# Performance work log

Hardware: AMD Instinct MI355X
Metric: run time of the kernel (lower is better)

## Reference

```python
import jax, jax.numpy as jnp
import numpy as np

MIN_NORM = 1e-15
EPS = 1e-5
C_CURV = 1.0  # args.c

def _norm(x):
    return jnp.clip(jnp.linalg.norm(x, axis=-1, keepdims=True), MIN_NORM)

def artanh(x):
    x = jnp.clip(x, -1.0 + EPS, 1.0 - EPS)
    return 0.5 * (jnp.log1p(x) - jnp.log1p(-x))

def proj(x, c):
    # clip points to stay strictly inside the Poincare ball
    norm = _norm(x)
    maxnorm = (1.0 - EPS) / jnp.sqrt(c)
    return jnp.where(norm > maxnorm, x / norm * maxnorm, x)

def expmap0(u, c):
    sqrt_c = jnp.sqrt(c)
    u_norm = _norm(u)
    return jnp.tanh(sqrt_c * u_norm) * u / (sqrt_c * u_norm)

def logmap0(p, c):
    sqrt_c = jnp.sqrt(c)
    p_norm = _norm(p)
    return artanh(sqrt_c * p_norm) * p / (sqrt_c * p_norm)

def mobius_add(x, y, c):
    x2 = jnp.sum(x * x, axis=-1, keepdims=True)
    y2 = jnp.sum(y * y, axis=-1, keepdims=True)
    xy = jnp.sum(x * y, axis=-1, keepdims=True)
    num = (1.0 + 2.0 * c * xy + c * y2) * x + (1.0 - c * x2) * y
    denom = 1.0 + 2.0 * c * xy + c * c * x2 * y2
    return num / jnp.clip(denom, MIN_NORM)

def mobius_matvec(W, x, c):
    sqrt_c = jnp.sqrt(c)
    x_norm = _norm(x)
    mx = x @ W.T
    mx_norm = _norm(mx)
    return jnp.tanh(mx_norm / x_norm * artanh(sqrt_c * x_norm)) * mx / (mx_norm * sqrt_c)

def poincare_dist(x, y, c):
    sqrt_c = jnp.sqrt(c)
    d = _norm(mobius_add(-x, y, c))[..., 0]
    return 2.0 / sqrt_c * artanh(sqrt_c * d)

def hgnn_layer(h, adj, W, b, c):
    # HypLinear: mobius matvec + hyperbolic bias
    mv = proj(mobius_matvec(W, h, c), c)
    hyp_b = proj(expmap0(b, c), c)
    h = proj(mobius_add(mv, hyp_b, c), c)
    # HypAgg: aggregate in tangent space at origin
    h = proj(expmap0(adj @ logmap0(h, c), c), c)
    # HypAct: relu in tangent space
    return proj(expmap0(jax.nn.relu(logmap0(h, c)), c), c)

def setup_inputs() -> dict:
    key = jax.random.key(0)
    ks = jax.random.split(key, 10)
    N, D, C, NC, NODE_C, L = 8192, 128, 64, 7, 7, 4
    x = jax.random.normal(ks[0], (N, D), jnp.float32)
    adj = jax.random.uniform(ks[1], (N, N), jnp.float32) / N  # row-stochastic-ish dense adjacency
    graph_indicator = jax.random.randint(ks[2], (N,), 0, 1)
    W_conv = jax.random.normal(ks[3], (L, D, D), jnp.float32) / np.sqrt(D)
    b_conv = jax.random.normal(ks[4], (L, D), jnp.float32) * 0.01
    centroids = jax.random.normal(ks[5], (C, D), jnp.float32) * 0.1
    W_mlp = jax.random.normal(ks[6], (NC, C), jnp.float32) * 0.1
    b_mlp = jnp.zeros((NC,), jnp.float32)
    W_mlp1 = jax.random.normal(ks[7], (NODE_C, D), jnp.float32) * 0.1
    b_mlp1 = jnp.zeros((NODE_C,), jnp.float32)
    return {"x": x, "adj": adj, "graph_indicator": graph_indicator,
            "W_conv": W_conv, "b_conv": b_conv, "centroids": centroids,
            "W_mlp": W_mlp, "b_mlp": b_mlp, "W_mlp1": W_mlp1, "b_mlp1": b_mlp1}

def reference(x, adj, graph_indicator, W_conv, b_conv, centroids, W_mlp, b_mlp, W_mlp1, b_mlp1):
    c = C_CURV
    # proj_tan0 is identity for PoincareBall
    h = proj(expmap0(x, c), c)
    # 2 residual blocks, each with 2 HGNN layers; shortcut is identity (in_dim == out_dim)
    for blk in range(2):
        res = h
        for j in range(2):
            idx = blk * 2 + j
            h = hgnn_layer(h, adj, W_conv[idx], b_conv[idx], c)
        h = h + res  # Euclidean residual, as in the source
    # CentroidDistance: pairwise hyperbolic distance [N, C]
    node_centroid_dist = poincare_dist(h[:, None, :], centroids[None, :, :], c)
    readout = jnp.mean(node_centroid_dist, axis=0, keepdims=True)  # [1, C]
    h_r = logmap0(readout, c)  # proj_tan0(logmap0(.)) -> identity proj_tan0
    logits = jax.nn.softmax(h_r @ W_mlp.T + b_mlp, axis=0)[None]        # [1,1,NC]
    h1 = logmap0(h, c)
    logits_node = jax.nn.softmax(h1 @ W_mlp1.T + b_mlp1, axis=0)[None]  # [1,N,node_classes]
    return (logits, logits_node, h_r)
```

## Files before the change

kernel.cpp:

```cpp
#include <hip/hip_runtime.h>

#define MIN_NORM 1e-15f
#define EPSV 1e-5f
#define MAXN (1.0f - EPSV)
#define NN 8192
#define DD 128

typedef unsigned short u16;
typedef __bf16 bf16x8 __attribute__((ext_vector_type(8)));
typedef float f32x4 __attribute__((ext_vector_type(4)));

__device__ __forceinline__ float wave_sum(float v) {
#pragma unroll
  for (int off = 32; off > 0; off >>= 1) v += __shfl_xor(v, off, 64);
  return v;
}

__device__ __forceinline__ float artanh_f(float x) {
  x = fminf(fmaxf(x, -1.0f + EPSV), 1.0f - EPSV);
  return 0.5f * (log1pf(x) - log1pf(-x));
}

__device__ __forceinline__ u16 f2bf(float f) {
  unsigned u = __float_as_uint(f);
  unsigned r = (u + 0x7fffu + ((u >> 16) & 1u)) >> 16;
  return (u16)r;
}
__device__ __forceinline__ float bf2f(u16 b) { return __uint_as_float(((unsigned)b) << 16); }

__device__ __forceinline__ void gload16(const u16* g, u16* l) {
  __builtin_amdgcn_global_load_lds((const __attribute__((address_space(1))) void*)(g),
                                   (__attribute__((address_space(3))) void*)(l), 16, 0, 0);
}

template <bool TILED>
__global__ __launch_bounds__(256) void gemm_bt(const u16* __restrict__ A,
                                               const u16* __restrict__ Bt,
                                               float* __restrict__ Cp,
                                               int M, int K, int KC) {
  __shared__ __align__(16) u16 Ash[2 * 64 * 64];
  __shared__ __align__(16) u16 Bsh[2 * 128 * 64];

  const int tid = threadIdx.x;
  const int lane = tid & 63;
  const int w = tid >> 6;
  const int wm = w >> 1, wn = w & 1;
  const int lrow = lane & 15;
  const int lq = lane >> 4;
  const int m0 = blockIdx.x * 64;
  const int kk0 = blockIdx.y * KC;
  const int kt0 = kk0 >> 6;
  const int bxK = blockIdx.x * (K >> 6);

  const int srow = lane >> 3;
  const int spc = lane & 7;

  const u16* Ap = A + (TILED ? 0 : (size_t)m0 * K);

  f32x4 acc[2][4];
#pragma unroll
  for (int a = 0; a < 2; a++)
#pragma unroll
    for (int b = 0; b < 4; b++)
#pragma unroll
      for (int r = 0; r < 4; r++) acc[a][b][r] = 0.0f;

#define STAGE(bf, tkt, kk)                                                     \
  do {                                                                         \
    if constexpr (TILED) {                                                     \
      const u16* at = A + (((size_t)(bxK + (tkt))) << 12) + (lane << 3);       \
      _Pragma("unroll") for (int ii = 0; ii < 2; ii++)                         \
        gload16(at + ((ii * 4 + w) << 9), &Ash[(bf) * 4096 + ((ii * 4 + w) << 9)]); \
      const u16* bt2 = Bt + (((size_t)(tkt)) << 13) + (lane << 3);             \
      _Pragma("unroll") for (int ii = 0; ii < 4; ii++)                         \
        gload16(bt2 + ((ii * 4 + w) << 9), &Bsh[(bf) * 8192 + ((ii * 4 + w) << 9)]); \
    } else {                                                                   \
      _Pragma("unroll") for (int ii = 0; ii < 2; ii++) {                       \
        int rw = ((ii * 4 + w) << 3) + srow;                                   \
        gload16(Ap + (size_t)rw * K + (kk) + ((spc ^ (rw & 7)) << 3),          \
                &Ash[(bf) * 4096 + ((ii * 4 + w) << 9)]);                      \
      }                                                                        \
      _Pragma("unroll") for (int ii = 0; ii < 4; ii++) {                       \
        int rw = ((ii * 4 + w) << 3) + srow;                                   \
        gload16(Bt + (size_t)rw * K + (kk) + ((spc ^ (rw & 7)) << 3),          \
                &Bsh[(bf) * 8192 + ((ii * 4 + w) << 9)]);                      \
      }                                                                        \
    }                                                                          \
  } while (0)

  const int nt = KC >> 6;
  STAGE(0, kt0, kk0);

  for (int t = 0; t < nt; t++) {
    const int cur = t & 1;
    __syncthreads();
    if (t + 1 < nt) STAGE(cur ^ 1, kt0 + t + 1, kk0 + (t + 1) * 64);

    const int abase = cur * 4096, bbase = cur * 8192;
#pragma unroll
    for (int ks = 0; ks < 2; ks++) {
      const int lc = ks * 4 + lq;
      bf16x8 af[2], bfr[4];
#pragma unroll
      for (int ti = 0; ti < 2; ti++) {
        int r = wm * 32 + ti * 16 + lrow;
        af[ti] = *(const bf16x8*)&Ash[abase + r * 64 + ((lc ^ (r & 7)) << 3)];
      }
#pragma unroll
      for (int tj = 0; tj < 4; tj++) {
        int n = wn * 64 + tj * 16 + lrow;
        bfr[tj] = *(const bf16x8*)&Bsh[bbase + n * 64 + ((lc ^ (n & 7)) << 3)];
      }
#pragma unroll
      for (int ti = 0; ti < 2; ti++)
#pragma unroll
        for (int tj = 0; tj < 4; tj++)
          acc[ti][tj] = __builtin_amdgcn_mfma_f32_16x16x32_bf16(af[ti], bfr[tj], acc[ti][tj], 0, 0, 0);
    }
  }
#undef STAGE

  float* C = Cp + (size_t)blockIdx.y * M * 128;
#pragma unroll
  for (int ti = 0; ti < 2; ti++)
#pragma unroll
    for (int tj = 0; tj < 4; tj++)
#pragma unroll
      for (int r = 0; r < 4; r++) {
        int row = m0 + wm * 32 + ti * 16 + lq * 4 + r;
        int col = wn * 64 + tj * 16 + lrow;
        C[(size_t)row * 128 + col] = acc[ti][tj][r];
      }
}

__global__ __launch_bounds__(256) void cvt_tile(const float* __restrict__ src,
                                                u16* __restrict__ dst) {
  int tid = threadIdx.x;
  int xb = blockIdx.x;
  int kg = blockIdx.y;
  int ch = tid & 63;
  int rs = tid >> 6;
#pragma unroll
  for (int rr = 0; rr < 16; rr++) {
    int row = rr * 4 + rs;
    int gk = kg * 512 + ch * 8;
    const float* s = src + (size_t)(xb * 64 + row) * NN + gk;
    float4 a = *(const float4*)s;
    float4 b = *(const float4*)(s + 4);
    ushort4 d0, d1;
    d0.x = f2bf(a.x); d0.y = f2bf(a.y); d0.z = f2bf(a.z); d0.w = f2bf(a.w);
    d1.x = f2bf(b.x); d1.y = f2bf(b.y); d1.z = f2bf(b.z); d1.w = f2bf(b.w);
    u16* d = dst + (((size_t)(xb * 128 + (gk >> 6))) << 12) + row * 64 +
             ((((gk >> 3) & 7) ^ (row & 7)) << 3);
    *(ushort4*)d = d0;
    *(ushort4*)(d + 4) = d1;
  }
}

__global__ void build_wt(const float* __restrict__ W, u16* __restrict__ Wt2) {
  int idx = blockIdx.x * 256 + threadIdx.x;
  if (idx >= 4 * 128 * 128) return;
  int layer = idx >> 14;
  int n = (idx >> 7) & 127;
  int k = idx & 127;
  float e = W[idx];
  u16 hi = f2bf(e);
  u16 lo = f2bf(e - bf2f(hi));
  u16* base = Wt2 + (size_t)layer * 128 * 384 + (size_t)n * 384;
  base[k] = hi;
  base[128 + k] = hi;
  base[256 + k] = lo;
}

__device__ __forceinline__ void write_split(u16* hs, int i, int lane, float v0, float v1) {
  u16* row = hs + (size_t)i * 384;
  u16 h0 = f2bf(v0), h1 = f2bf(v1);
  u16 l0 = f2bf(v0 - bf2f(h0)), l1 = f2bf(v1 - bf2f(h1));
  row[lane] = h0;         row[lane + 64] = h1;
  row[128 + lane] = l0;   row[128 + 64 + lane] = l1;
  row[256 + lane] = h0;   row[256 + 64 + lane] = h1;
}

__global__ __launch_bounds__(64) void rowwise_init(const float* __restrict__ x,
                                                   float* __restrict__ h,
                                                   float* __restrict__ res,
                                                   u16* __restrict__ hsplit) {
  int i = blockIdx.x, lane = threadIdx.x;
  const float* xr = x + (size_t)i * DD;
  float a0 = xr[lane], a1 = xr[lane + 64];
  float n = fmaxf(sqrtf(wave_sum(a0 * a0 + a1 * a1)), MIN_NORM);
  float g = tanhf(n) / n;
  float y0 = g * a0, y1 = g * a1;
  float pn = fmaxf(sqrtf(wave_sum(y0 * y0 + y1 * y1)), MIN_NORM);
  float s = pn > MAXN ? MAXN / pn : 1.0f;
  y0 *= s; y1 *= s;
  size_t base = (size_t)i * DD;
  h[base + lane] = y0;   h[base + lane + 64] = y1;
  res[base + lane] = y0; res[base + lane + 64] = y1;
  write_split(hsplit, i, lane, y0, y1);
}

__global__ __launch_bounds__(64) void rowwise_mid(const float* __restrict__ h,
                                                  const float* __restrict__ P,
                                                  const float* __restrict__ bvec,
                                                  u16* __restrict__ uT2) {
  int i = blockIdx.x, lane = threadIdx.x;
  size_t base = (size_t)i * DD;
  const float* hr = h + base;
  float h0 = hr[lane], h1 = hr[lane + 64];
  float m0 = 0.f, m1 = 0.f;
#pragma unroll
  for (int sk = 0; sk < 3; sk++) {
    const float* p = P + (size_t)sk * NN * DD + base;
    m0 += p[lane];
    m1 += p[lane + 64];
  }
  float xn = fmaxf(sqrtf(wave_sum(h0 * h0 + h1 * h1)), MIN_NORM);
  float mn = fmaxf(sqrtf(wave_sum(m0 * m0 + m1 * m1)), MIN_NORM);
  float t = tanhf(mn / xn * artanh_f(xn));
  float v0 = t * m0 / mn, v1 = t * m1 / mn;
  float pn = fmaxf(sqrtf(wave_sum(v0 * v0 + v1 * v1)), MIN_NORM);
  float sc = pn > MAXN ? MAXN / pn : 1.0f;
  v0 *= sc; v1 *= sc;
  float b0 = bvec[lane], b1 = bvec[lane + 64];
  float bn = fmaxf(sqrtf(wave_sum(b0 * b0 + b1 * b1)), MIN_NORM);
  float gb = tanhf(bn) / bn;
  float e0 = gb * b0, e1 = gb * b1;
  float en = fmaxf(sqrtf(wave_sum(e0 * e0 + e1 * e1)), MIN_NORM);
  float sb = en > MAXN ? MAXN / en : 1.0f;
  e0 *= sb; e1 *= sb;
  float x2 = wave_sum(v0 * v0 + v1 * v1);
  float y2 = wave_sum(e0 * e0 + e1 * e1);
  float xy = wave_sum(v0 * e0 + v1 * e1);
  float ca = 1.0f + 2.0f * xy + y2;
  float cb = 1.0f - x2;
  float den = fmaxf(1.0f + 2.0f * xy + x2 * y2, MIN_NORM);
  float t0 = (ca * v0 + cb * e0) / den, t1 = (ca * v1 + cb * e1) / den;
  float tn = fmaxf(sqrtf(wave_sum(t0 * t0 + t1 * t1)), MIN_NORM);
  float st = tn > MAXN ? MAXN / tn : 1.0f;
  t0 *= st; t1 *= st;
  float pn2 = fmaxf(sqrtf(wave_sum(t0 * t0 + t1 * t1)), MIN_NORM);
  float gl = artanh_f(pn2) / pn2;
  u16* tb = uT2 + (((size_t)(i >> 6)) << 13);
  int c8 = (i >> 3) & 7, k7 = i & 7;
  tb[lane * 64 + (((c8) ^ (lane & 7)) << 3) + k7] = f2bf(gl * t0);
  int n2 = lane + 64;
  tb[n2 * 64 + (((c8) ^ (n2 & 7)) << 3) + k7] = f2bf(gl * t1);
}

__global__ __launch_bounds__(64) void rowwise_post(const float* __restrict__ P,
                                                   float* __restrict__ h,
                                                   float* __restrict__ res,
                                                   u16* __restrict__ hsplit,
                                                   int addres) {
  int i = blockIdx.x, lane = threadIdx.x;
  size_t base = (size_t)i * DD;
  float m0 = 0.f, m1 = 0.f;
#pragma unroll
  for (int sk = 0; sk < 8; sk++) {
    const float* p = P + (size_t)sk * NN * DD + base;
    m0 += p[lane];
    m1 += p[lane + 64];
  }
  float n = fmaxf(sqrtf(wave_sum(m0 * m0 + m1 * m1)), MIN_NORM);
  float g = tanhf(n) / n;
  float y0 = g * m0, y1 = g * m1;
  float pn = fmaxf(sqrtf(wave_sum(y0 * y0 + y1 * y1)), MIN_NORM);
  float s = pn > MAXN ? MAXN / pn : 1.0f;
  y0 *= s; y1 *= s;
  float hn = fmaxf(sqrtf(wave_sum(y0 * y0 + y1 * y1)), MIN_NORM);
  float gl = artanh_f(hn) / hn;
  float u0 = fmaxf(gl * y0, 0.0f), u1 = fmaxf(gl * y1, 0.0f);
  float un = fmaxf(sqrtf(wave_sum(u0 * u0 + u1 * u1)), MIN_NORM);
  float ge = tanhf(un) / un;
  float z0 = ge * u0, z1 = ge * u1;
  float zn = fmaxf(sqrtf(wave_sum(z0 * z0 + z1 * z1)), MIN_NORM);
  float sz = zn > MAXN ? MAXN / zn : 1.0f;
  z0 *= sz; z1 *= sz;
  if (addres) {
    z0 += res[base + lane];
    z1 += res[base + lane + 64];
    res[base + lane] = z0;
    res[base + lane + 64] = z1;
  }
  h[base + lane] = z0;
  h[base + lane + 64] = z1;
  write_split(hsplit, i, lane, z0, z1);
}

__global__ __launch_bounds__(256) void centroid_k(const float* __restrict__ h,
                                                  const float* __restrict__ cen,
                                                  float* __restrict__ rs) {
  __shared__ float cs[64 * 129];
  __shared__ float hs[32 * 128];
  __shared__ float y2s[64];
  int tid = threadIdx.x;
  int i0 = blockIdx.x * 32;
  for (int idx = tid; idx < 64 * 128; idx += 256) {
    int r = idx >> 7, c = idx & 127;
    cs[r * 129 + c] = cen[idx];
  }
  for (int idx = tid; idx < 32 * 128; idx += 256) hs[idx] = h[(size_t)i0 * 128 + idx];
  __syncthreads();
  if (tid < 64) {
    float s = 0.f;
    for (int k = 0; k < 128; k++) { float v = cs[tid * 129 + k]; s = fmaf(v, v, s); }
    y2s[tid] = s;
  }
  __syncthreads();
  int w = tid >> 6, lane = tid & 63;
  float dsum = 0.f;
  for (int rr = 0; rr < 8; rr++) {
    int r = w * 8 + rr;
    float dot = 0.f, x2 = 0.f;
    for (int k = 0; k < 128; k++) {
      float hk = hs[r * 128 + k];
      dot = fmaf(hk, cs[lane * 129 + k], dot);
      x2 = fmaf(hk, hk, x2);
    }
    float y2 = y2s[lane];
    float al = 1.0f - 2.0f * dot + y2;
    float be = 1.0f - x2;
    float num2 = al * al * x2 + be * be * y2 - 2.0f * al * be * dot;
    float den = fmaxf(1.0f - 2.0f * dot + x2 * y2, MIN_NORM);
    float d = fmaxf(sqrtf(fmaxf(num2, 0.0f)) / den, MIN_NORM);
    dsum += 2.0f * artanh_f(d);
  }
  atomicAdd(&rs[lane], dsum);
}

__global__ __launch_bounds__(64) void finalize_k(const float* __restrict__ rs,
                                                 float* __restrict__ out) {
  int lane = threadIdx.x;
  float r = rs[lane] * (1.0f / 8192.0f);
  float n = fmaxf(sqrtf(wave_sum(r * r)), MIN_NORM);
  float a = artanh_f(n);
  out[7 + NN * 7 + lane] = a * r / n;
  if (lane < 7) out[lane] = 1.0f;
}

__global__ __launch_bounds__(64) void scores_k(const float* __restrict__ h,
                                               const float* __restrict__ Wm,
                                               const float* __restrict__ bm,
                                               float* __restrict__ sc) {
  int i = blockIdx.x, lane = threadIdx.x;
  const float* hr = h + (size_t)i * DD;
  float h0 = hr[lane], h1 = hr[lane + 64];
  float pn = fmaxf(sqrtf(wave_sum(h0 * h0 + h1 * h1)), MIN_NORM);
  float gl = artanh_f(pn) / pn;
  float u0 = gl * h0, u1 = gl * h1;
  float p[7];
#pragma unroll
  for (int j = 0; j < 7; j++)
    p[j] = wave_sum(u0 * Wm[j * 128 + lane] + u1 * Wm[j * 128 + lane + 64]);
  float v = p[0];
#pragma unroll
  for (int j = 1; j < 7; j++)
    if (lane == j) v = p[j];
  if (lane < 7) sc[(size_t)i * 7 + lane] = v + bm[lane];
}

__global__ __launch_bounds__(256) void softmax_col(const float* __restrict__ sc,
                                                   float* __restrict__ out) {
  __shared__ float buf[256][8];
  int tid = threadIdx.x;
  float mx[7];
#pragma unroll
  for (int j = 0; j < 7; j++) mx[j] = -1e30f;
  for (int i = tid; i < NN; i += 256)
#pragma unroll
    for (int j = 0; j < 7; j++) mx[j] = fmaxf(mx[j], sc[i * 7 + j]);
#pragma unroll
  for (int j = 0; j < 7; j++) buf[tid][j] = mx[j];
  __syncthreads();
  for (int off = 128; off > 0; off >>= 1) {
    if (tid < off)
#pragma unroll
      for (int j = 0; j < 7; j++) buf[tid][j] = fmaxf(buf[tid][j], buf[tid + off][j]);
    __syncthreads();
  }
  float cm[7];
#pragma unroll
  for (int j = 0; j < 7; j++) cm[j] = buf[0][j];
  __syncthreads();
  float sm[7];
#pragma unroll
  for (int j = 0; j < 7; j++) sm[j] = 0.f;
  for (int i = tid; i < NN; i += 256)
#pragma unroll
    for (int j = 0; j < 7; j++) sm[j] += expf(sc[i * 7 + j] - cm[j]);
#pragma unroll
  for (int j = 0; j < 7; j++) buf[tid][j] = sm[j];
  __syncthreads();
  for (int off = 128; off > 0; off >>= 1) {
    if (tid < off)
#pragma unroll
      for (int j = 0; j < 7; j++) buf[tid][j] += buf[tid + off][j];
    __syncthreads();
  }
  float csum[7];
#pragma unroll
  for (int j = 0; j < 7; j++) csum[j] = buf[0][j];
  __syncthreads();
  for (int idx = tid; idx < NN * 7; idx += 256) {
    int i = idx / 7, j = idx - i * 7;
    out[idx] = expf(sc[i * 7 + j] - cm[j]) / csum[j];
  }
}

extern "C" void kernel_launch(void* const* d_in, const int* in_sizes, int n_in,
                              void* d_out, int out_size, void* d_ws, size_t ws_size,
                              hipStream_t stream) {
  const float* x = (const float*)d_in[0];
  const float* adj = (const float*)d_in[1];
  const float* W_conv = (const float*)d_in[3];
  const float* b_conv = (const float*)d_in[4];
  const float* centroids = (const float*)d_in[5];
  const float* W_mlp1 = (const float*)d_in[8];
  const float* b_mlp1 = (const float*)d_in[9];
  float* out = (float*)d_out;

  char* ws = (char*)d_ws;
  size_t off = 0;
  auto alloc = [&](size_t bytes) {
    void* p = ws + off;
    off = (off + bytes + 255) & ~(size_t)255;
    return p;
  };
  float* h = (float*)alloc((size_t)NN * DD * 4);
  float* res = (float*)alloc((size_t)NN * DD * 4);
  u16* hsplit = (u16*)alloc((size_t)NN * 384 * 2);
  u16* uT2 = (u16*)alloc((size_t)DD * NN * 2);
  u16* Wt2 = (u16*)alloc((size_t)4 * 128 * 384 * 2);
  float* P = (float*)alloc((size_t)8 * NN * DD * 4);
  u16* adjT = (u16*)alloc((size_t)NN * NN * 2);
  float* scores = (float*)alloc((size_t)NN * 7 * 4);
  float* rs = (float*)alloc(64 * 4);
  (void)ws_size; (void)in_sizes; (void)n_in; (void)out_size;

  hipMemsetAsync(rs, 0, 64 * 4, stream);
  build_wt<<<(4 * 128 * 128 + 255) / 256, 256, 0, stream>>>(W_conv, Wt2);
  rowwise_init<<<NN, 64, 0, stream>>>(x, h, res, hsplit);
  cvt_tile<<<dim3(128, 16), 256, 0, stream>>>(adj, adjT);
  for (int layer = 0; layer < 4; layer++) {
    gemm_bt<false><<<dim3(NN / 64, 3), 256, 0, stream>>>(
        hsplit, Wt2 + (size_t)layer * 128 * 384, P, NN, 384, 128);
    rowwise_mid<<<NN, 64, 0, stream>>>(h, P, b_conv + layer * DD, uT2);
    gemm_bt<true><<<dim3(NN / 64, 8), 256, 0, stream>>>(
        adjT, uT2, P, NN, NN, NN / 8);
    rowwise_post<<<NN, 64, 0, stream>>>(P, h, res, hsplit, (layer & 1));
  }
  centroid_k<<<256, 256, 0, stream>>>(h, centroids, rs);
  finalize_k<<<1, 64, 0, stream>>>(rs, out);
  scores_k<<<NN, 64, 0, stream>>>(h, W_mlp1, b_mlp1, scores);
  softmax_col<<<1, 256, 0, stream>>>(scores, out + 7);
}
```

Measured before the change: 811.9 us.

## Triple-buffer GEMM LDS staging with partial vmcnt waits

Moves the bf16 GEMM main loop from double buffering to a three-stage LDS ring. Tile t+2 is prefetched while tile t is computed, and a partial s_waitcnt vmcnt(6) replaces the full __syncthreads drain. The aim is to keep more global-to-LDS loads in flight and hide memory latency behind the MFMA work. LDS use grows by half, which may cut occupancy. The hand-counted vmcnt value and the single barrier per iteration are fragile: if the count is wrong, the code reads a buffer before its load has finished, or races on a buffer that is being overwritten.

```diff
diff --git a/kernel.cpp b/kernel.cpp
--- a/kernel.cpp
+++ b/kernel.cpp
@@ -38,8 +38,8 @@
                                                const u16* __restrict__ Bt,
                                                float* __restrict__ Cp,
                                                int M, int K, int KC) {
-  __shared__ __align__(16) u16 Ash[2 * 64 * 64];
-  __shared__ __align__(16) u16 Bsh[2 * 128 * 64];
+  __shared__ __align__(16) u16 Ash[3 * 64 * 64];
+  __shared__ __align__(16) u16 Bsh[3 * 128 * 64];
 
   const int tid = threadIdx.x;
   const int lane = tid & 63;
@@ -88,37 +88,44 @@
     }                                                                          \
   } while (0)
 
+#define COMPUTE(bf)                                                            \
+  do {                                                                         \
+    const int abase = (bf) * 4096, bbase = (bf) * 8192;                        \
+    _Pragma("unroll") for (int ks = 0; ks < 2; ks++) {                         \
+      const int lc = ks * 4 + lq;                                              \
+      bf16x8 af[2], bfr[4];                                                    \
+      _Pragma("unroll") for (int ti = 0; ti < 2; ti++) {                       \
+        int r = wm * 32 + ti * 16 + lrow;                                      \
+        af[ti] = *(const bf16x8*)&Ash[abase + r * 64 + ((lc ^ (r & 7)) << 3)]; \
+      }                                                                        \
+      _Pragma("unroll") for (int tj = 0; tj < 4; tj++) {                       \
+        int n = wn * 64 + tj * 16 + lrow;                                      \
+        bfr[tj] = *(const bf16x8*)&Bsh[bbase + n * 64 + ((lc ^ (n & 7)) << 3)]; \
+      }                                                                        \
+      _Pragma("unroll") for (int ti = 0; ti < 2; ti++)                         \
+        _Pragma("unroll") for (int tj = 0; tj < 4; tj++)                       \
+          acc[ti][tj] = __builtin_amdgcn_mfma_f32_16x16x32_bf16(af[ti], bfr[tj], acc[ti][tj], 0, 0, 0); \
+    }                                                                          \
+  } while (0)
+
   const int nt = KC >> 6;
   STAGE(0, kt0, kk0);
-
-  for (int t = 0; t < nt; t++) {
-    const int cur = t & 1;
-    __syncthreads();
-    if (t + 1 < nt) STAGE(cur ^ 1, kt0 + t + 1, kk0 + (t + 1) * 64);
-
-    const int abase = cur * 4096, bbase = cur * 8192;
-#pragma unroll
-    for (int ks = 0; ks < 2; ks++) {
-      const int lc = ks * 4 + lq;
-      bf16x8 af[2], bfr[4];
-#pragma unroll
-      for (int ti = 0; ti < 2; ti++) {
-        int r = wm * 32 + ti * 16 + lrow;
-        af[ti] = *(const bf16x8*)&Ash[abase + r * 64 + ((lc ^ (r & 7)) << 3)];
-      }
-#pragma unroll
-      for (int tj = 0; tj < 4; tj++) {
-        int n = wn * 64 + tj * 16 + lrow;
-        bfr[tj] = *(const bf16x8*)&Bsh[bbase + n * 64 + ((lc ^ (n & 7)) << 3)];
-      }
-#pragma unroll
-      for (int ti = 0; ti < 2; ti++)
-#pragma unroll
-        for (int tj = 0; tj < 4; tj++)
-          acc[ti][tj] = __builtin_amdgcn_mfma_f32_16x16x32_bf16(af[ti], bfr[tj], acc[ti][tj], 0, 0, 0);
+  if (nt > 1) STAGE(1, kt0 + 1, kk0 + 64);
+
+  for (int t = 0; t < nt - 1; t++) {
+    asm volatile("s_waitcnt vmcnt(6)" ::: "memory");
+    __builtin_amdgcn_s_barrier();
+    if (t + 2 < nt) {
+      const int b2 = (t + 2) % 3;
+      STAGE(b2, kt0 + t + 2, kk0 + (t + 2) * 64);
     }
-  }
+    COMPUTE(t % 3);
+  }
+  asm volatile("s_waitcnt vmcnt(0)" ::: "memory");
+  __builtin_amdgcn_s_barrier();
+  COMPUTE((nt - 1) % 3);
 #undef STAGE
+#undef COMPUTE
 
   float* C = Cp + (size_t)blockIdx.y * M * 128;
 #pragma unroll
```

After: 812.5 us. Within noise of the previous version (+0.1%).
